# Optimization experiments

Hardware: AMD Instinct MI355X
Metric: run time of the kernel (lower is better)

The kernel has to match this reference:

```python
import jax, jax.numpy as jnp
import numpy as np

B_, L_, DIN, DM, DS, DR, K = 2, 1024, 1024, 2048, 16, 128, 4


def setup_inputs() -> dict:
    key = jax.random.key(0)
    ks = jax.random.split(key, 10)
    s = lambda k, shape, sc=0.02: (jax.random.normal(k, shape, jnp.float32) * sc)
    A_init = jnp.tile(jnp.arange(1, DS + 1, dtype=jnp.float32)[None, :], (DM, 1))  # (DM, DS)
    return {
        'x_in': jax.random.normal(ks[0], (B_, L_, DIN), jnp.float32),
        'W_in': s(ks[1], (DIN, DM)),
        'W_res': s(ks[2], (DIN, DM)),
        'W_out': s(ks[3], (DM, DIN)),
        'conv_w': s(ks[4], (DM, K), 0.1),   # depthwise conv weight (torch shape (DM,1,K) squeezed)
        'conv_b': jnp.zeros((DM,), jnp.float32),
        'A_log': jnp.log(A_init),
        'D': jnp.ones((DM,), jnp.float32),
        'W_B': s(ks[5], (DM, DS)),
        'W_C': s(ks[6], (DM, DS)),
        'W_dt': s(ks[7], (DM, DR)),
        'dt_w': s(ks[8], (DR, DM)),
        'dt_b': jnp.zeros((DM,), jnp.float32),
    }


def reference(x_in, W_in, W_res, W_out, conv_w, conv_b, A_log, D, W_B, W_C, W_dt, dt_w, dt_b):
    Bb, L, _ = x_in.shape
    x = x_in @ W_in                     # (B, L, DM)
    res = x_in @ W_res                  # (B, L, DM)
    # Causal depthwise conv1d: pad left k-1, truncate to L (matches Conv1d(padding=k-1)[:, :, :L])
    xp = jnp.pad(x, ((0, 0), (K - 1, 0), (0, 0)))
    xc = conv_b
    for i in range(K):
        xc = xc + xp[:, i:i + L, :] * conv_w[:, i]
    xc = jax.nn.silu(xc)                # (B, L, DM)
    # Selective SSM (fused_ssm)
    A = -jnp.exp(A_log)                 # (DM, DS)
    Bp = xc @ W_B                       # (B, L, DS)
    Cp = xc @ W_C                       # (B, L, DS)
    delta = jax.nn.softplus((xc @ W_dt) @ dt_w + dt_b)  # (B, L, DM)
    dA = jnp.exp(delta[..., None] * A)                       # (B, L, DM, DS)
    dBu = delta[..., None] * Bp[:, :, None, :] * xc[..., None]  # (B, L, DM, DS)

    def step(h, inp):
        dA_t, dBu_t, C_t = inp
        h = dA_t * h + dBu_t                         # (B, DM, DS)
        y = jnp.einsum('bdn,bn->bd', h, C_t)         # (B, DM)
        return h, y

    h0 = jnp.zeros((Bb, DM, DS), jnp.float32)
    _, ys = jax.lax.scan(step, h0, (dA.transpose(1, 0, 2, 3), dBu.transpose(1, 0, 2, 3), Cp.transpose(1, 0, 2)))
    y = ys.transpose(1, 0, 2) + D * xc  # (B, L, DM)
    y = y * jax.nn.silu(res)
    return y @ W_out                    # (B, L, DIN)
```

## Files before the change

kernel.cpp:

```cpp
#include <hip/hip_runtime.h>
#include <hip/hip_bf16.h>

constexpr int B_  = 2;
constexpr int L_  = 1024;
constexpr int DIN = 1024;
constexpr int DM  = 2048;
constexpr int DS  = 16;
constexpr int DR  = 128;
constexpr int KC  = 4;
constexpr int M_  = B_ * L_;
constexpr int NP2 = 256;
constexpr int NPC = 160;
constexpr int KSLICES = 8;
constexpr int KSL = DM / KSLICES;

constexpr int NC = 32;
constexpr int CL = L_ / NC;
constexpr int S_ = B_ * DM * DS;

typedef __bf16 bf16x8 __attribute__((ext_vector_type(8)));
typedef float  f32x4  __attribute__((ext_vector_type(4)));

__device__ __forceinline__ void gload_lds16(const void* g, void* l) {
    __builtin_amdgcn_global_load_lds(
        (const __attribute__((address_space(1))) void*)g,
        (__attribute__((address_space(3))) void*)l, 16, 0, 0);
}

__device__ __forceinline__ void transpose_block(const float* __restrict__ in,
                                                __bf16* __restrict__ out,
                                                int R, int C, int bx, int by, int t) {
    __shared__ float tile[32][33];
    int tx = t & 31, ty = t >> 5;
    #pragma unroll
    for (int j = 0; j < 32; j += 8)
        tile[ty + j][tx] = in[(size_t)(by * 32 + ty + j) * C + (bx * 32 + tx)];
    __syncthreads();
    #pragma unroll
    for (int j = 0; j < 32; j += 8)
        out[(size_t)(bx * 32 + ty + j) * R + (by * 32 + tx)] = (__bf16)tile[tx][ty + j];
}

__global__ void prep_all(const float* __restrict__ x_in, const float* __restrict__ W_in,
                         const float* __restrict__ W_res, const float* __restrict__ W_out,
                         const float* __restrict__ dt_w,
                         const float* __restrict__ W_B, const float* __restrict__ W_C,
                         const float* __restrict__ W_dt, const float* __restrict__ conv_w,
                         __bf16* __restrict__ xinB, __bf16* __restrict__ WinT,
                         __bf16* __restrict__ WresT, __bf16* __restrict__ WoutT,
                         __bf16* __restrict__ dtwT, __bf16* __restrict__ projW,
                         float* __restrict__ cwT, float* __restrict__ outz) {
    int blk = blockIdx.x, t = threadIdx.x;
    if (blk < 8192) {
        int i = blk * 256 + t;
        xinB[i] = (__bf16)x_in[i];
    } else if (blk < 10240) {
        int b = blk - 8192;
        transpose_block(W_in, WinT, DIN, DM, b % 64, b / 64, t);
    } else if (blk < 12288) {
        int b = blk - 10240;
        transpose_block(W_res, WresT, DIN, DM, b % 64, b / 64, t);
    } else if (blk < 14336) {
        int b = blk - 12288;
        transpose_block(W_out, WoutT, DM, DIN, b % 32, b / 32, t);
    } else if (blk < 14592) {
        int b = blk - 14336;
        transpose_block(dt_w, dtwT, DR, DM, b % 64, b / 64, t);
    } else if (blk < 16640) {
        int i = (blk - 14592) * 256 + t;
        int k = i % DM;
        int n = i / DM;
        float v = 0.f;
        if (n < 16)        v = W_B[(size_t)k * DS + n];
        else if (n < 32)   v = W_C[(size_t)k * DS + (n - 16)];
        else if (n < 160)  v = W_dt[(size_t)k * DR + (n - 32)];
        projW[i] = (__bf16)v;
    } else if (blk < 16672) {
        int j = (blk - 16640) * 256 + t;
        int tap = j / DM, d = j % DM;
        cwT[j] = conv_w[d * KC + tap];
    } else {
        int i = (blk - 16672) * 256 + t;
        ((f32x4*)outz)[i] = f32x4{0.f, 0.f, 0.f, 0.f};
    }
}

__global__ void reduce_split(const __bf16* __restrict__ PpartB, float* __restrict__ Bp,
                             float* __restrict__ Cp, __bf16* __restrict__ dtmpB) {
    int i = blockIdx.x * 256 + threadIdx.x;
    int row = i / NPC, c = i % NPC;
    float v = 0.f;
    #pragma unroll
    for (int ks = 0; ks < KSLICES; ks++)
        v += (float)PpartB[(size_t)ks * M_ * NPC + i];
    if (c < 16)       Bp[(size_t)row * DS + c] = v;
    else if (c < 32)  Cp[(size_t)row * DS + (c - 16)] = v;
    else              dtmpB[(size_t)row * DR + (c - 32)] = (__bf16)v;
}

template<int EPI>
__global__ __launch_bounds__(1024, 8)
void gemm_tile128(const __bf16* __restrict__ A, const __bf16* __restrict__ BT,
                  float* __restrict__ Cf, __bf16* __restrict__ Cb,
                  const float* __restrict__ bias, int M, int N, int K,
                  int lda, int ldb) {
    __shared__ __bf16 sA[2][2][128 * 32];
    __shared__ __bf16 sB[2][2][128 * 32];
    int t = threadIdx.x;
    int lane = t & 63, w = t >> 6;
    int wm = w >> 2, wn = w & 3;
    int m0 = blockIdx.y * 128, n0 = blockIdx.x * 128;
    int kbase = blockIdx.z * K;
    int q = lane >> 4, rr = lane & 15;

    f32x4 acc[2][2] = {};

    const int nt = K >> 6;

    int t2 = t & 511;
    int srow = t2 >> 2;
    int slot = t2 & 3;
    int gkb = slot ^ ((srow >> 1) & 3);

    auto stage = [&](int kt, int bufi) {
        if (t < 512) {
            #pragma unroll
            for (int s = 0; s < 2; s++)
                gload_lds16(A + (size_t)(m0 + srow) * lda + kbase + kt + s * 32 + gkb * 8,
                            &sA[bufi][s][w * 512]);
        } else {
            #pragma unroll
            for (int s = 0; s < 2; s++)
                gload_lds16(BT + (size_t)(n0 + srow) * ldb + kbase + kt + s * 32 + gkb * 8,
                            &sB[bufi][s][(w - 8) * 512]);
        }
    };

    stage(0, 0);
    __syncthreads();

    int cur = 0;
    for (int tix = 0; tix < nt; tix++) {
        if (tix + 1 < nt) stage((tix + 1) << 6, cur ^ 1);

        #pragma unroll
        for (int s = 0; s < 2; s++) {
            bf16x8 af[2], bfr[2];
            #pragma unroll
            for (int i = 0; i < 2; i++) {
                int rowA = wm * 32 + i * 16 + rr;
                af[i] = *(const bf16x8*)(&sA[cur][s][rowA * 32 + ((q ^ ((rowA >> 1) & 3)) * 8)]);
            }
            #pragma unroll
            for (int j = 0; j < 2; j++) {
                int rowB = wn * 32 + j * 16 + rr;
                bfr[j] = *(const bf16x8*)(&sB[cur][s][rowB * 32 + ((q ^ ((rowB >> 1) & 3)) * 8)]);
            }
            #pragma unroll
            for (int i = 0; i < 2; i++)
                #pragma unroll
                for (int j = 0; j < 2; j++)
                    acc[i][j] = __builtin_amdgcn_mfma_f32_16x16x32_bf16(af[i], bfr[j], acc[i][j], 0, 0, 0);
        }

        __syncthreads();
        cur ^= 1;
    }

    #pragma unroll
    for (int i = 0; i < 2; i++) {
        #pragma unroll
        for (int j = 0; j < 2; j++) {
            int col = n0 + wn * 32 + j * 16 + rr;
            #pragma unroll
            for (int jj = 0; jj < 4; jj++) {
                int row = m0 + wm * 32 + i * 16 + q * 4 + jj;
                float v = acc[i][j][jj];
                if (EPI == 1) {
                    float z = v + bias[col];
                    Cb[(size_t)row * N + col] = (__bf16)((z > 20.f) ? z : log1pf(__expf(z)));
                } else if (EPI == 2) {
                    if (col < DM) ((__bf16*)Cf)[(size_t)row * DM + col] = (__bf16)v;
                    else          Cb[(size_t)row * DM + (col - DM)] = (__bf16)v;
                } else {
                    if (col < NPC)
                        Cb[(size_t)blockIdx.z * M * NPC + (size_t)row * NPC + col] = (__bf16)v;
                }
            }
        }
    }
}

__global__ void gemm_out64(const __bf16* __restrict__ A, const __bf16* __restrict__ BT,
                           float* __restrict__ C, int M, int N, int K, int lda, int ldb) {
    __shared__ __bf16 sA[2][2][128 * 32];
    __shared__ __bf16 sB[2][2][64 * 32];
    int t = threadIdx.x;
    int lane = t & 63, w = t >> 6;
    int wm = w >> 1, wn = w & 1;
    int m0 = blockIdx.y * 128, n0 = blockIdx.x * 64;
    int kh = K >> 1;
    int kbase = blockIdx.z * kh;
    int q = lane >> 4, rr = lane & 15;

    f32x4 acc[2][2] = {};
    int srow = t >> 2;
    int slot = t & 3;

    const int nt = kh >> 6;

    auto stage = [&](int kt, int bufi) {
        int gkb = slot ^ ((srow >> 1) & 3);
        #pragma unroll
        for (int s = 0; s < 2; s++) {
            gload_lds16(A + (size_t)(m0 + srow) * lda + kbase + kt + s * 32 + gkb * 8,
                        &sA[bufi][s][w * 512]);
            if (t < 256)
                gload_lds16(BT + (size_t)(n0 + srow) * ldb + kbase + kt + s * 32 + gkb * 8,
                            &sB[bufi][s][w * 512]);
        }
    };

    stage(0, 0);
    __syncthreads();

    int cur = 0;
    for (int tix = 0; tix < nt; tix++) {
        if (tix + 1 < nt) stage((tix + 1) << 6, cur ^ 1);

        #pragma unroll
        for (int s = 0; s < 2; s++) {
            bf16x8 af[2], bfr[2];
            #pragma unroll
            for (int i = 0; i < 2; i++) {
                int rowA = wm * 32 + i * 16 + rr;
                af[i] = *(const bf16x8*)(&sA[cur][s][rowA * 32 + ((q ^ ((rowA >> 1) & 3)) * 8)]);
            }
            #pragma unroll
            for (int j = 0; j < 2; j++) {
                int rowB = wn * 32 + j * 16 + rr;
                bfr[j] = *(const bf16x8*)(&sB[cur][s][rowB * 32 + ((q ^ ((rowB >> 1) & 3)) * 8)]);
            }
            #pragma unroll
            for (int i = 0; i < 2; i++)
                #pragma unroll
                for (int j = 0; j < 2; j++)
                    acc[i][j] = __builtin_amdgcn_mfma_f32_16x16x32_bf16(af[i], bfr[j], acc[i][j], 0, 0, 0);
        }

        __syncthreads();
        cur ^= 1;
    }

    #pragma unroll
    for (int i = 0; i < 2; i++) {
        #pragma unroll
        for (int j = 0; j < 2; j++) {
            int col = n0 + wn * 32 + j * 16 + rr;
            #pragma unroll
            for (int jj = 0; jj < 4; jj++) {
                int row = m0 + wm * 32 + i * 16 + q * 4 + jj;
                atomicAdd(&C[(size_t)row * N + col], acc[i][j][jj]);
            }
        }
    }
}

__global__ void conv_silu(const __bf16* __restrict__ x, const float* __restrict__ cwT,
                          const float* __restrict__ bias, __bf16* __restrict__ xcB) {
    int row = blockIdx.x;
    int d   = threadIdx.x * 8;
    int l   = row % L_;
    size_t base = (size_t)row * DM + d;

    float acc[8];
    {
        const f32x4* b4 = (const f32x4*)(bias + d);
        f32x4 b0 = b4[0], b1 = b4[1];
        #pragma unroll
        for (int q = 0; q < 4; q++) { acc[q] = b0[q]; acc[4 + q] = b1[q]; }
    }
    #pragma unroll
    for (int i = 0; i < KC; i++) {
        int li = l - (KC - 1) + i;
        if (li >= 0) {
            bf16x8 xv = *(const bf16x8*)(x + base + (size_t)(i - (KC - 1)) * DM);
            const f32x4* w4 = (const f32x4*)(cwT + (size_t)i * DM + d);
            f32x4 w0 = w4[0], w1 = w4[1];
            #pragma unroll
            for (int q = 0; q < 4; q++) {
                acc[q]     = fmaf((float)xv[q],     w0[q], acc[q]);
                acc[4 + q] = fmaf((float)xv[4 + q], w1[q], acc[4 + q]);
            }
        }
    }
    bf16x8 out;
    #pragma unroll
    for (int q = 0; q < 8; q++) {
        float v = acc[q] / (1.f + __expf(-acc[q]));
        out[q] = (__bf16)v;
    }
    *(bf16x8*)(xcB + base) = out;
}

__global__ void scan_phase1(const __bf16* __restrict__ delta, const __bf16* __restrict__ xc,
                            const float* __restrict__ Bp, const float* __restrict__ A_log,
                            __bf16* __restrict__ aprodB, __bf16* __restrict__ cendB) {
    int blk = blockIdx.x;
    int c   = blk % NC;
    int rem = blk / NC;
    int dmt = rem % (DM / 256);
    int b   = rem / (DM / 256);
    int t   = threadIdx.x;
    int dm  = dmt * 256 + t;
    int l0  = c * CL;

    __shared__ float sB[CL * DS];
    sB[t]       = Bp[((size_t)b * L_ + l0) * DS + t];
    sB[t + 256] = Bp[((size_t)b * L_ + l0) * DS + t + 256];
    __syncthreads();

    float Aval[DS];
    {
        const f32x4* Ap = (const f32x4*)(A_log + (size_t)dm * DS);
        #pragma unroll
        for (int r4 = 0; r4 < 4; r4++) {
            f32x4 a = Ap[r4];
            #pragma unroll
            for (int q = 0; q < 4; q++) Aval[r4 * 4 + q] = -__expf(a[q]);
        }
    }

    float h[DS], ap[DS];
    #pragma unroll
    for (int i = 0; i < DS; i++) { h[i] = 0.f; ap[i] = 1.f; }

    size_t base = ((size_t)b * L_ + l0) * DM + dm;
    #pragma unroll 4
    for (int j = 0; j < CL; j++) {
        float dl  = (float)delta[base + (size_t)j * DM];
        float xv  = (float)xc[base + (size_t)j * DM];
        float cmn = dl * xv;
        const f32x4* sB4 = (const f32x4*)(sB + j * DS);
        #pragma unroll
        for (int r4 = 0; r4 < 4; r4++) {
            f32x4 bv = sB4[r4];
            #pragma unroll
            for (int q = 0; q < 4; q++) {
                int i = r4 * 4 + q;
                float dA = __expf(dl * Aval[i]);
                ap[i] *= dA;
                h[i] = fmaf(dA, h[i], cmn * bv[q]);
            }
        }
    }

    size_t s = ((size_t)(b * DM + dm)) * DS;
    #pragma unroll
    for (int r8 = 0; r8 < 2; r8++) {
        bf16x8 va, vh;
        #pragma unroll
        for (int q = 0; q < 8; q++) { va[q] = (__bf16)ap[r8 * 8 + q]; vh[q] = (__bf16)h[r8 * 8 + q]; }
        ((bf16x8*)(aprodB + (size_t)c * S_ + s))[r8] = va;
        ((bf16x8*)(cendB  + (size_t)c * S_ + s))[r8] = vh;
    }
}

__global__ void scan_phase2(const __bf16* __restrict__ aprodB, const __bf16* __restrict__ cendB,
                            __bf16* __restrict__ hinitB) {
    int u = blockIdx.x * 256 + threadIdx.x;
    float h = 0.f;
    #pragma unroll
    for (int c = 0; c < NC; c++) {
        float a  = (float)aprodB[(size_t)c * S_ + u];
        float ce = (float)cendB [(size_t)c * S_ + u];
        hinitB[(size_t)c * S_ + u] = (__bf16)h;
        h = fmaf(a, h, ce);
    }
}

__global__ void scan_phase3(const __bf16* __restrict__ delta, const __bf16* __restrict__ xc,
                            const float* __restrict__ Bp, const float* __restrict__ Cp,
                            const __bf16* __restrict__ res, const float* __restrict__ A_log,
                            const float* __restrict__ Dw, const __bf16* __restrict__ hinitB,
                            __bf16* __restrict__ ybar) {
    int blk = blockIdx.x;
    int c   = blk % NC;
    int rem = blk / NC;
    int dmt = rem % (DM / 256);
    int b   = rem / (DM / 256);
    int t   = threadIdx.x;
    int dm  = dmt * 256 + t;
    int l0  = c * CL;

    __shared__ float sB[CL * DS];
    __shared__ float sC[CL * DS];
    sB[t]       = Bp[((size_t)b * L_ + l0) * DS + t];
    sB[t + 256] = Bp[((size_t)b * L_ + l0) * DS + t + 256];
    sC[t]       = Cp[((size_t)b * L_ + l0) * DS + t];
    sC[t + 256] = Cp[((size_t)b * L_ + l0) * DS + t + 256];
    __syncthreads();

    float Aval[DS];
    {
        const f32x4* Ap = (const f32x4*)(A_log + (size_t)dm * DS);
        #pragma unroll
        for (int r4 = 0; r4 < 4; r4++) {
            f32x4 a = Ap[r4];
            #pragma unroll
            for (int q = 0; q < 4; q++) Aval[r4 * 4 + q] = -__expf(a[q]);
        }
    }
    float Dval = Dw[dm];

    float h[DS];
    {
        size_t s = ((size_t)(b * DM + dm)) * DS;
        #pragma unroll
        for (int r8 = 0; r8 < 2; r8++) {
            bf16x8 v = ((const bf16x8*)(hinitB + (size_t)c * S_ + s))[r8];
            #pragma unroll
            for (int q = 0; q < 8; q++) h[r8 * 8 + q] = (float)v[q];
        }
    }

    size_t base = ((size_t)b * L_ + l0) * DM + dm;
    #pragma unroll 4
    for (int j = 0; j < CL; j++) {
        float dl  = (float)delta[base + (size_t)j * DM];
        float xv  = (float)xc[base + (size_t)j * DM];
        float rv  = (float)res[base + (size_t)j * DM];
        float cmn = dl * xv;
        float y = 0.f;
        const f32x4* sB4 = (const f32x4*)(sB + j * DS);
        const f32x4* sC4 = (const f32x4*)(sC + j * DS);
        #pragma unroll
        for (int r4 = 0; r4 < 4; r4++) {
            f32x4 bv = sB4[r4];
            f32x4 cv = sC4[r4];
            #pragma unroll
            for (int q = 0; q < 4; q++) {
                int i = r4 * 4 + q;
                float dA = __expf(dl * Aval[i]);
                h[i] = fmaf(dA, h[i], cmn * bv[q]);
                y = fmaf(h[i], cv[q], y);
            }
        }
        float g = rv / (1.f + __expf(-rv));
        ybar[base + (size_t)j * DM] = (__bf16)((y + Dval * xv) * g);
    }
}

extern "C" void kernel_launch(void* const* d_in, const int* in_sizes, int n_in,
                              void* d_out, int out_size, void* d_ws, size_t ws_size,
                              hipStream_t stream) {
    const float* x_in   = (const float*)d_in[0];
    const float* W_in   = (const float*)d_in[1];
    const float* W_res  = (const float*)d_in[2];
    const float* W_out  = (const float*)d_in[3];
    const float* conv_w = (const float*)d_in[4];
    const float* conv_b = (const float*)d_in[5];
    const float* A_log  = (const float*)d_in[6];
    const float* Dw     = (const float*)d_in[7];
    const float* W_B    = (const float*)d_in[8];
    const float* W_C    = (const float*)d_in[9];
    const float* W_dt   = (const float*)d_in[10];
    const float* dt_w   = (const float*)d_in[11];
    const float* dt_b   = (const float*)d_in[12];

    float* ws_f = (float*)d_ws;
    float* Bp    = ws_f;
    float* Cp    = Bp + (size_t)M_ * DS;
    float* cwT   = Cp + (size_t)M_ * DS;
    __bf16* bf_base = (__bf16*)(cwT + (size_t)KC * DM);
    __bf16* ybar   = bf_base;
    __bf16* xinB   = ybar   + (size_t)M_ * DM;
    __bf16* WinT   = xinB   + (size_t)M_ * DIN;
    __bf16* WresT  = WinT   + (size_t)DM * DIN;
    __bf16* WoutT  = WresT  + (size_t)DM * DIN;
    __bf16* xB     = WoutT  + (size_t)DIN * DM;
    __bf16* xcB    = xB     + (size_t)M_ * DM;
    __bf16* projW  = xcB    + (size_t)M_ * DM;
    __bf16* dtwT   = projW  + (size_t)NP2 * DM;
    __bf16* dtmpB  = dtwT   + (size_t)DM * DR;
    __bf16* deltaB = dtmpB  + (size_t)M_ * DR;
    __bf16* resB   = deltaB + (size_t)M_ * DM;
    __bf16* aprodB = resB   + (size_t)M_ * DM;
    __bf16* cendB  = aprodB + (size_t)NC * S_;
    __bf16* hinitB = cendB  + (size_t)NC * S_;
    __bf16* PpartB = hinitB + (size_t)NC * S_;

    prep_all<<<18720, 256, 0, stream>>>(x_in, W_in, W_res, W_out, dt_w, W_B, W_C, W_dt,
                                        conv_w, xinB, WinT, WresT, WoutT, dtwT, projW,
                                        cwT, (float*)d_out);

    gemm_tile128<2><<<dim3((2 * DM) / 128, M_ / 128, 1), 1024, 0, stream>>>(
        xinB, WinT, (float*)xB, resB, nullptr, M_, 2 * DM, DIN, DIN, DIN);

    conv_silu<<<M_, 256, 0, stream>>>(xB, cwT, conv_b, xcB);

    gemm_tile128<4><<<dim3(NP2 / 128, M_ / 128, KSLICES), 1024, 0, stream>>>(
        xcB, projW, nullptr, PpartB, nullptr, M_, NP2, KSL, DM, DM);
    reduce_split<<<(M_ * NPC) / 256, 256, 0, stream>>>(PpartB, Bp, Cp, dtmpB);

    gemm_tile128<1><<<dim3(DM / 128, M_ / 128, 1), 1024, 0, stream>>>(
        dtmpB, dtwT, nullptr, deltaB, dt_b, M_, DM, DR, DR, DR);

    int nblk = B_ * (DM / 256) * NC;
    scan_phase1<<<nblk, 256, 0, stream>>>(deltaB, xcB, Bp, A_log, aprodB, cendB);
    scan_phase2<<<S_ / 256, 256, 0, stream>>>(aprodB, cendB, hinitB);
    scan_phase3<<<nblk, 256, 0, stream>>>(deltaB, xcB, Bp, Cp, resB, A_log, Dw, hinitB, ybar);

    gemm_out64<<<dim3(DIN / 64, M_ / 128, 2), 512, 0, stream>>>(
        ybar, WoutT, (float*)d_out, M_, DIN, DM, DM, DM);
}
```

Measured before the change: 245.4 us.

## Fuse causal conv and SiLU into input GEMM epilogue with halo recompute

Replaces the separate x/res input GEMM and conv_silu kernel with one kernel. It computes the 128-row x tile plus a 16-row halo through extra MFMAs, stages the result in LDS, and applies the 4-tap causal depthwise conv and SiLU before writing xc. This removes the bf16 round trip of x through global memory and one launch, at the cost of redundant halo MFMAs, lower occupancy, and rounding x to bf16 in LDS. The prep kernel also now converts x_in with 4-wide vector loads and stores.

After: 242.0 us. No clear change (-1.4%).

```diff
diff --git a/kernel.cpp b/kernel.cpp
--- a/kernel.cpp
+++ b/kernel.cpp
@@ -19,6 +19,7 @@
 constexpr int S_ = B_ * DM * DS;
 
 typedef __bf16 bf16x8 __attribute__((ext_vector_type(8)));
+typedef __bf16 bf16x4 __attribute__((ext_vector_type(4)));
 typedef float  f32x4  __attribute__((ext_vector_type(4)));
 
 __device__ __forceinline__ void gload_lds16(const void* g, void* l) {
@@ -51,23 +52,27 @@
                          __bf16* __restrict__ dtwT, __bf16* __restrict__ projW,
                          float* __restrict__ cwT, float* __restrict__ outz) {
     int blk = blockIdx.x, t = threadIdx.x;
-    if (blk < 8192) {
-        int i = blk * 256 + t;
-        xinB[i] = (__bf16)x_in[i];
-    } else if (blk < 10240) {
+    if (blk < 2048) {
+        int i4 = blk * 256 + t;
+        f32x4 v = ((const f32x4*)x_in)[i4];
+        bf16x4 o;
+        #pragma unroll
+        for (int q = 0; q < 4; q++) o[q] = (__bf16)v[q];
+        ((bf16x4*)xinB)[i4] = o;
+    } else if (blk < 4096) {
+        int b = blk - 2048;
+        transpose_block(W_in, WinT, DIN, DM, b % 64, b / 64, t);
+    } else if (blk < 6144) {
+        int b = blk - 4096;
+        transpose_block(W_res, WresT, DIN, DM, b % 64, b / 64, t);
+    } else if (blk < 8192) {
+        int b = blk - 6144;
+        transpose_block(W_out, WoutT, DM, DIN, b % 32, b / 32, t);
+    } else if (blk < 8448) {
         int b = blk - 8192;
-        transpose_block(W_in, WinT, DIN, DM, b % 64, b / 64, t);
-    } else if (blk < 12288) {
-        int b = blk - 10240;
-        transpose_block(W_res, WresT, DIN, DM, b % 64, b / 64, t);
-    } else if (blk < 14336) {
-        int b = blk - 12288;
-        transpose_block(W_out, WoutT, DM, DIN, b % 32, b / 32, t);
-    } else if (blk < 14592) {
-        int b = blk - 14336;
         transpose_block(dt_w, dtwT, DR, DM, b % 64, b / 64, t);
-    } else if (blk < 16640) {
-        int i = (blk - 14592) * 256 + t;
+    } else if (blk < 10496) {
+        int i = (blk - 8448) * 256 + t;
         int k = i % DM;
         int n = i / DM;
         float v = 0.f;
@@ -75,12 +80,12 @@
         else if (n < 32)   v = W_C[(size_t)k * DS + (n - 16)];
         else if (n < 160)  v = W_dt[(size_t)k * DR + (n - 32)];
         projW[i] = (__bf16)v;
-    } else if (blk < 16672) {
-        int j = (blk - 16640) * 256 + t;
+    } else if (blk < 10528) {
+        int j = (blk - 10496) * 256 + t;
         int tap = j / DM, d = j % DM;
         cwT[j] = conv_w[d * KC + tap];
     } else {
-        int i = (blk - 16672) * 256 + t;
+        int i = (blk - 10528) * 256 + t;
         ((f32x4*)outz)[i] = f32x4{0.f, 0.f, 0.f, 0.f};
     }
 }
@@ -98,12 +103,166 @@
     else              dtmpB[(size_t)row * DR + (c - 32)] = (__bf16)v;
 }
 
+__global__ __launch_bounds__(1024, 4)
+void gemm_in_conv(const __bf16* __restrict__ A, const __bf16* __restrict__ BT,
+                  __bf16* __restrict__ xcB, __bf16* __restrict__ resB,
+                  const float* __restrict__ cwT, const float* __restrict__ conv_b) {
+    __shared__ __bf16 smem[32768];
+    const int lda = DIN, ldb = DIN, K = DIN;
+    int t = threadIdx.x;
+    int lane = t & 63, w = t >> 6;
+    int wm = w >> 2, wn = w & 3;
+    int m0 = blockIdx.y * 128, n0 = blockIdx.x * 128;
+    int q = lane >> 4, rr = lane & 15;
+    bool is_x = (n0 < DM);
+    bool has_halo = is_x && ((m0 & (L_ - 1)) != 0);
+
+    f32x4 acc[2][2] = {};
+    f32x4 hacc[2] = {};
+
+    const int nt = K >> 6;
+
+    int t2 = t & 511;
+    int srow = t2 >> 2;
+    int slot = t2 & 3;
+    int gkb = slot ^ ((srow >> 1) & 3);
+
+    auto SA = [&](int buf, int s) { return smem + (buf * 2 + s) * 4096; };
+    auto SB = [&](int buf, int s) { return smem + 16384 + (buf * 2 + s) * 4096; };
+
+    auto stage = [&](int kt, int bufi) {
+        if (t < 512) {
+            #pragma unroll
+            for (int s = 0; s < 2; s++)
+                gload_lds16(A + (size_t)(m0 + srow) * lda + kt + s * 32 + gkb * 8,
+                            SA(bufi, s) + w * 512);
+        } else {
+            #pragma unroll
+            for (int s = 0; s < 2; s++)
+                gload_lds16(BT + (size_t)(n0 + srow) * ldb + kt + s * 32 + gkb * 8,
+                            SB(bufi, s) + (w - 8) * 512);
+        }
+    };
+
+    bf16x8 ah[2];
+    if (wm == 0 && has_halo) {
+        #pragma unroll
+        for (int s = 0; s < 2; s++)
+            ah[s] = *(const bf16x8*)(A + (size_t)(m0 - 16 + rr) * lda + s * 32 + q * 8);
+    }
+
+    stage(0, 0);
+    __syncthreads();
+
+    int cur = 0;
+    for (int tix = 0; tix < nt; tix++) {
+        if (tix + 1 < nt) stage((tix + 1) << 6, cur ^ 1);
+
+        bf16x8 ahn[2];
+        if (wm == 0 && has_halo && tix + 1 < nt) {
+            int ktn = (tix + 1) << 6;
+            #pragma unroll
+            for (int s = 0; s < 2; s++)
+                ahn[s] = *(const bf16x8*)(A + (size_t)(m0 - 16 + rr) * lda + ktn + s * 32 + q * 8);
+        }
+
+        #pragma unroll
+        for (int s = 0; s < 2; s++) {
+            bf16x8 af[2], bfr[2];
+            #pragma unroll
+            for (int i = 0; i < 2; i++) {
+                int rowA = wm * 32 + i * 16 + rr;
+                af[i] = *(const bf16x8*)(SA(cur, s) + rowA * 32 + ((q ^ ((rowA >> 1) & 3)) * 8));
+            }
+            #pragma unroll
+            for (int j = 0; j < 2; j++) {
+                int rowB = wn * 32 + j * 16 + rr;
+                bfr[j] = *(const bf16x8*)(SB(cur, s) + rowB * 32 + ((q ^ ((rowB >> 1) & 3)) * 8));
+            }
+            #pragma unroll
+            for (int i = 0; i < 2; i++)
+                #pragma unroll
+                for (int j = 0; j < 2; j++)
+                    acc[i][j] = __builtin_amdgcn_mfma_f32_16x16x32_bf16(af[i], bfr[j], acc[i][j], 0, 0, 0);
+            if (wm == 0 && has_halo) {
+                hacc[0] = __builtin_amdgcn_mfma_f32_16x16x32_bf16(ah[s], bfr[0], hacc[0], 0, 0, 0);
+                hacc[1] = __builtin_amdgcn_mfma_f32_16x16x32_bf16(ah[s], bfr[1], hacc[1], 0, 0, 0);
+            }
+        }
+        if (wm == 0 && has_halo && tix + 1 < nt) { ah[0] = ahn[0]; ah[1] = ahn[1]; }
+
+        __syncthreads();
+        cur ^= 1;
+    }
+
+    if (!is_x) {
+        #pragma unroll
+        for (int i = 0; i < 2; i++) {
+            #pragma unroll
+            for (int j = 0; j < 2; j++) {
+                int col = (n0 - DM) + wn * 32 + j * 16 + rr;
+                #pragma unroll
+                for (int jj = 0; jj < 4; jj++) {
+                    int row = m0 + wm * 32 + i * 16 + q * 4 + jj;
+                    resB[(size_t)row * DM + col] = (__bf16)acc[i][j][jj];
+                }
+            }
+        }
+        return;
+    }
+
+    constexpr int XS = 136;
+    #pragma unroll
+    for (int i = 0; i < 2; i++)
+        #pragma unroll
+        for (int j = 0; j < 2; j++) {
+            int cc = wn * 32 + j * 16 + rr;
+            #pragma unroll
+            for (int jj = 0; jj < 4; jj++) {
+                int r = wm * 32 + i * 16 + q * 4 + jj;
+                smem[(r + 3) * XS + cc] = (__bf16)acc[i][j][jj];
+            }
+        }
+    if (wm == 0) {
+        #pragma unroll
+        for (int j = 0; j < 2; j++) {
+            int cc = wn * 32 + j * 16 + rr;
+            #pragma unroll
+            for (int jj = 0; jj < 4; jj++) {
+                int r = q * 4 + jj;
+                if (r >= 13)
+                    smem[(r - 13) * XS + cc] = has_halo ? (__bf16)hacc[j][jj] : (__bf16)0.f;
+            }
+        }
+    }
+    __syncthreads();
+
+    {
+        int c  = t & 127;
+        int rg = t >> 7;
+        int d  = n0 + c;
+        float w0 = cwT[0 * DM + d], w1 = cwT[1 * DM + d];
+        float w2 = cwT[2 * DM + d], w3 = cwT[3 * DM + d];
+        float bv = conv_b[d];
+        float x0 = (float)smem[(rg * 16 + 0) * XS + c];
+        float x1 = (float)smem[(rg * 16 + 1) * XS + c];
+        float x2 = (float)smem[(rg * 16 + 2) * XS + c];
+        #pragma unroll
+        for (int k = 0; k < 16; k++) {
+            float x3 = (float)smem[(rg * 16 + k + 3) * XS + c];
+            float v = fmaf(x3, w3, fmaf(x2, w2, fmaf(x1, w1, fmaf(x0, w0, bv))));
+            float sv = v / (1.f + __expf(-v));
+            xcB[(size_t)(m0 + rg * 16 + k) * DM + d] = (__bf16)sv;
+            x0 = x1; x1 = x2; x2 = x3;
+        }
+    }
+}
+
 template<int EPI>
 __global__ __launch_bounds__(1024, 8)
 void gemm_tile128(const __bf16* __restrict__ A, const __bf16* __restrict__ BT,
-                  float* __restrict__ Cf, __bf16* __restrict__ Cb,
-                  const float* __restrict__ bias, int M, int N, int K,
-                  int lda, int ldb) {
+                  __bf16* __restrict__ Cb, const float* __restrict__ bias,
+                  int M, int N, int K, int lda, int ldb) {
     __shared__ __bf16 sA[2][2][128 * 32];
     __shared__ __bf16 sB[2][2][128 * 32];
     int t = threadIdx.x;
@@ -179,9 +338,6 @@
                 if (EPI == 1) {
                     float z = v + bias[col];
                     Cb[(size_t)row * N + col] = (__bf16)((z > 20.f) ? z : log1pf(__expf(z)));
-                } else if (EPI == 2) {
-                    if (col < DM) ((__bf16*)Cf)[(size_t)row * DM + col] = (__bf16)v;
-                    else          Cb[(size_t)row * DM + (col - DM)] = (__bf16)v;
                 } else {
                     if (col < NPC)
                         Cb[(size_t)blockIdx.z * M * NPC + (size_t)row * NPC + col] = (__bf16)v;
@@ -264,43 +420,6 @@
             }
         }
     }
-}
-
-__global__ void conv_silu(const __bf16* __restrict__ x, const float* __restrict__ cwT,
-                          const float* __restrict__ bias, __bf16* __restrict__ xcB) {
-    int row = blockIdx.x;
-    int d   = threadIdx.x * 8;
-    int l   = row % L_;
-    size_t base = (size_t)row * DM + d;
-
-    float acc[8];
-    {
-        const f32x4* b4 = (const f32x4*)(bias + d);
-        f32x4 b0 = b4[0], b1 = b4[1];
-        #pragma unroll
-        for (int q = 0; q < 4; q++) { acc[q] = b0[q]; acc[4 + q] = b1[q]; }
-    }
-    #pragma unroll
-    for (int i = 0; i < KC; i++) {
-        int li = l - (KC - 1) + i;
-        if (li >= 0) {
-            bf16x8 xv = *(const bf16x8*)(x + base + (size_t)(i - (KC - 1)) * DM);
-            const f32x4* w4 = (const f32x4*)(cwT + (size_t)i * DM + d);
-            f32x4 w0 = w4[0], w1 = w4[1];
-            #pragma unroll
-            for (int q = 0; q < 4; q++) {
-                acc[q]     = fmaf((float)xv[q],     w0[q], acc[q]);
-                acc[4 + q] = fmaf((float)xv[4 + q], w1[q], acc[4 + q]);
-            }
-        }
-    }
-    bf16x8 out;
-    #pragma unroll
-    for (int q = 0; q < 8; q++) {
-        float v = acc[q] / (1.f + __expf(-acc[q]));
-        out[q] = (__bf16)v;
-    }
-    *(bf16x8*)(xcB + base) = out;
 }
 
 __global__ void scan_phase1(const __bf16* __restrict__ delta, const __bf16* __restrict__ xc,
@@ -490,21 +609,19 @@
     __bf16* hinitB = cendB  + (size_t)NC * S_;
     __bf16* PpartB = hinitB + (size_t)NC * S_;
 
-    prep_all<<<18720, 256, 0, stream>>>(x_in, W_in, W_res, W_out, dt_w, W_B, W_C, W_dt,
+    prep_all<<<12576, 256, 0, stream>>>(x_in, W_in, W_res, W_out, dt_w, W_B, W_C, W_dt,
                                         conv_w, xinB, WinT, WresT, WoutT, dtwT, projW,
                                         cwT, (float*)d_out);
 
-    gemm_tile128<2><<<dim3((2 * DM) / 128, M_ / 128, 1), 1024, 0, stream>>>(
-        xinB, WinT, (float*)xB, resB, nullptr, M_, 2 * DM, DIN, DIN, DIN);
-
-    conv_silu<<<M_, 256, 0, stream>>>(xB, cwT, conv_b, xcB);
+    gemm_in_conv<<<dim3((2 * DM) / 128, M_ / 128), 1024, 0, stream>>>(
+        xinB, WinT, xcB, resB, cwT, conv_b);
 
     gemm_tile128<4><<<dim3(NP2 / 128, M_ / 128, KSLICES), 1024, 0, stream>>>(
-        xcB, projW, nullptr, PpartB, nullptr, M_, NP2, KSL, DM, DM);
+        xcB, projW, PpartB, nullptr, M_, NP2, KSL, DM, DM);
     reduce_split<<<(M_ * NPC) / 256, 256, 0, stream>>>(PpartB, Bp, Cp, dtmpB);
 
     gemm_tile128<1><<<dim3(DM / 128, M_ / 128, 1), 1024, 0, stream>>>(
-        dtmpB, dtwT, nullptr, deltaB, dt_b, M_, DM, DR, DR, DR);
+        dtmpB, dtwT, deltaB, dt_b, M_, DM, DR, DR, DR);
 
     int nblk = B_ * (DM / 256) * NC;
     scan_phase1<<<nblk, 256, 0, stream>>>(deltaB, xcB, Bp, A_log, aprodB, cendB);
```
